# Kernel optimization log

Hardware: AMD Instinct MI355X
Metric: run time of the kernel (lower is better)

The kernel has to match this reference:

```python
import jax, jax.numpy as jnp
import numpy as np

IN_C = 256
OUT_C = 256
N = 100000
E = 3200000


def setup_inputs() -> dict:
    key = jax.random.key(0)
    ks = jax.random.split(key, 8)
    x = jax.random.normal(ks[0], (N, IN_C), dtype=jnp.float32)
    edge_index = jax.random.randint(ks[1], (2, E), 0, N, dtype=jnp.int64)
    # GCNConv weights (glorot-scale) and biases
    s1 = float(np.sqrt(2.0 / (IN_C + OUT_C)))
    s2 = float(np.sqrt(2.0 / (OUT_C + OUT_C)))
    W1 = jax.random.normal(ks[2], (IN_C, OUT_C), dtype=jnp.float32) * s1
    b1 = jnp.zeros((OUT_C,), dtype=jnp.float32)
    W2 = jax.random.normal(ks[3], (OUT_C, OUT_C), dtype=jnp.float32) * s2
    b2 = jnp.zeros((OUT_C,), dtype=jnp.float32)
    alpha = jnp.asarray(0.25, dtype=jnp.float32)  # PReLU default init
    return {"x": x, "edge_index": edge_index, "W1": W1, "b1": b1,
            "W2": W2, "b2": b2, "alpha": alpha}


def _gcn_aggregate(h, src, dst, norm, b, n):
    # message = norm_e * h[src_e]; scatter-add into dst; add bias
    msg = h[src] * norm[:, None]
    agg = jax.ops.segment_sum(msg, dst, num_segments=n)
    return agg + b


def reference(x, edge_index, W1, b1, W2, b2, alpha):
    n = x.shape[0]
    loops = jnp.arange(n, dtype=edge_index.dtype)
    src = jnp.concatenate([edge_index[0], loops])  # self-loops appended
    dst = jnp.concatenate([edge_index[1], loops])
    # symmetric degree normalization with self-loops (PyG GCNConv default)
    deg = jax.ops.segment_sum(jnp.ones_like(dst, dtype=x.dtype), dst, num_segments=n)
    dis = jnp.where(deg > 0, jax.lax.rsqrt(jnp.maximum(deg, 1e-12)), 0.0)
    norm = dis[src] * dis[dst]
    # layer 1: linear -> normalized scatter-aggregate -> PReLU
    h = _gcn_aggregate(x @ W1, src, dst, norm, b1, n)
    h = jnp.where(h >= 0, h, alpha * h)
    # layer 2 (last layer, no activation; batch=None -> node embeddings)
    h = _gcn_aggregate(h @ W2, src, dst, norm, b2, n)
    return h
```

## Files before the change

kernel.cpp:

```cpp
#include <hip/hip_runtime.h>
#include <cstdint>
#include <cstddef>


#define IN_C 256
#define BSHIFT 9
#define BCAP 24576

typedef __attribute__((ext_vector_type(8))) short bf16x8;
typedef __attribute__((ext_vector_type(4))) float f32x4;

__device__ __forceinline__ ushort f2bf(float x) {
    union { float f; uint32_t u; } v; v.f = x;
    uint32_t r = v.u + 0x7FFF + ((v.u >> 16) & 1);
    return (ushort)(r >> 16);
}
__device__ __forceinline__ float bf2f(ushort b) {
    union { uint32_t u; float f; } v; v.u = ((uint32_t)b) << 16;
    return v.f;
}

__global__ __launch_bounds__(256) void passA(const int* __restrict__ ei,
                                             int* __restrict__ bucketCnt,
                                             int2* __restrict__ bucketBuf, int E, int NB) {
    __shared__ int hist[256];
    __shared__ int gbase[256];
    __shared__ int cur[256];
    int tid = threadIdx.x;
    hist[tid] = 0; cur[tid] = 0;
    __syncthreads();
    int e0 = blockIdx.x * 4096;
    int src_r[16], dst_r[16];
#pragma unroll
    for (int i = 0; i < 16; ++i) {
        int e = e0 + i * 256 + tid;
        if (e < E) {
            src_r[i] = ei[e];
            dst_r[i] = ei[(size_t)E + e];
            atomicAdd(&hist[dst_r[i] >> BSHIFT], 1);
        } else dst_r[i] = -1;
    }
    __syncthreads();
    if (tid < NB && hist[tid] > 0) gbase[tid] = atomicAdd(&bucketCnt[tid], hist[tid]);
    __syncthreads();
#pragma unroll
    for (int i = 0; i < 16; ++i) {
        if (dst_r[i] >= 0) {
            int b = dst_r[i] >> BSHIFT;
            int p = atomicAdd(&cur[b], 1);
            int pos = gbase[b] + p;
            if (pos < BCAP) bucketBuf[(size_t)b * BCAP + pos] = make_int2(src_r[i], dst_r[i]);
        }
    }
}

__global__ void bucket_scan(const int* __restrict__ bucketCnt, int* __restrict__ bucket_base,
                            int* __restrict__ row_ptr, int NB, int N) {
    if (threadIdx.x == 0 && blockIdx.x == 0) {
        int run = 0;
        for (int b = 0; b < NB; ++b) {
            int c = bucketCnt[b]; if (c > BCAP) c = BCAP;
            bucket_base[b] = run; run += c;
        }
        row_ptr[N] = run;
    }
}

__global__ __launch_bounds__(256) void passB(const int2* __restrict__ bucketBuf,
                                             const int* __restrict__ bucketCnt,
                                             const int* __restrict__ bucket_base,
                                             int* __restrict__ row_ptr,
                                             int* __restrict__ csr_src, int N) {
    __shared__ int cnt[512];
    __shared__ int ofs[512];
    __shared__ int ssum[256];
    int b = blockIdx.x, tid = threadIdx.x;
    int base_node = b << BSHIFT;
    int nnodes = N - base_node; if (nnodes > 512) nnodes = 512;
    int nE = bucketCnt[b]; if (nE > BCAP) nE = BCAP;
    const int2* buf = bucketBuf + (size_t)b * BCAP;
    cnt[tid] = 0; cnt[tid + 256] = 0;
    __syncthreads();
    for (int i = tid; i < nE; i += 256) {
        int2 p = buf[i];
        atomicAdd(&cnt[p.y - base_node], 1);
    }
    __syncthreads();
    int c0 = cnt[2 * tid], c1 = cnt[2 * tid + 1];
    int s = c0 + c1;
    ssum[tid] = s;
    __syncthreads();
    for (int o = 1; o < 256; o <<= 1) {
        int add = (tid >= o) ? ssum[tid - o] : 0;
        __syncthreads();
        ssum[tid] += add;
        __syncthreads();
    }
    int run = ssum[tid] - s;
    int gb = bucket_base[b];
    int o0 = gb + run, o1 = gb + run + c0;
    ofs[2 * tid] = o0; ofs[2 * tid + 1] = o1;
    if (2 * tid < nnodes)     row_ptr[base_node + 2 * tid]     = o0;
    if (2 * tid + 1 < nnodes) row_ptr[base_node + 2 * tid + 1] = o1;
    __syncthreads();
    for (int i = tid; i < nE; i += 256) {
        int2 p = buf[i];
        int pos = atomicAdd(&ofs[p.y - base_node], 1);
        csr_src[pos] = p.x;
    }
}

__global__ __launch_bounds__(256) void dis2(const int* __restrict__ row_ptr,
                                            float* __restrict__ dis, int N) {
    int i = blockIdx.x * 256 + threadIdx.x;
    if (i < N) dis[i] = rsqrtf((float)(row_ptr[i + 1] - row_ptr[i] + 1));
}

__global__ __launch_bounds__(256) void split_x(const float* __restrict__ x,
                                               ushort* __restrict__ Xh,
                                               ushort* __restrict__ Xl, int total4) {
    int id = blockIdx.x * 256 + threadIdx.x;
    if (id >= total4) return;
    float4 v = ((const float4*)x)[id];
    ushort hx = f2bf(v.x), hy = f2bf(v.y), hz = f2bf(v.z), hw = f2bf(v.w);
    ((ushort4*)Xh)[id] = make_ushort4(hx, hy, hz, hw);
    ((ushort4*)Xl)[id] = make_ushort4(f2bf(v.x - bf2f(hx)), f2bf(v.y - bf2f(hy)),
                                      f2bf(v.z - bf2f(hz)), f2bf(v.w - bf2f(hw)));
}

__global__ __launch_bounds__(256) void prep_w(const float* __restrict__ W,
                                              ushort* __restrict__ WTh,
                                              ushort* __restrict__ WTl) {
    int id = blockIdx.x * 256 + threadIdx.x;
    int n = id >> 8, k = id & 255;
    float w = W[k * 256 + n];
    ushort h = f2bf(w);
    WTh[id] = h;
    WTl[id] = f2bf(w - bf2f(h));
}

__global__ __launch_bounds__(512, 2) void gemm_lds(const ushort* __restrict__ Ah,
                                                   const ushort* __restrict__ Al,
                                                   const ushort* __restrict__ Bh,
                                                   const ushort* __restrict__ Bl,
                                                   const float* __restrict__ dis,
                                                   ushort* __restrict__ C, int M) {
    __shared__ ushort Bsh[128][264];
    __shared__ ushort Bsl[128][264];
    int tid = threadIdx.x;
    int col0 = (blockIdx.x & 1) << 7;
    int brow = (blockIdx.x >> 1) << 9;
#pragma unroll
    for (int i = 0; i < 8; ++i) {
        int u = tid + i * 512;
        int cb = u >> 5, ko = (u & 31) * 8;
        *(bf16x8*)&Bsh[cb][ko] = *(const bf16x8*)&Bh[(size_t)(col0 + cb) * 256 + ko];
        *(bf16x8*)&Bsl[cb][ko] = *(const bf16x8*)&Bl[(size_t)(col0 + cb) * 256 + ko];
    }
    __syncthreads();

    int wave = tid >> 6, lane = tid & 63;
    int row0 = brow + wave * 64;
    if (row0 >= M) return;
    int lrow = lane & 15, lk = (lane >> 4) * 8;

    f32x4 acc[4][8];
#pragma unroll
    for (int i = 0; i < 4; ++i)
#pragma unroll
        for (int j = 0; j < 8; ++j) acc[i][j] = (f32x4)0.f;

#pragma unroll
    for (int ks = 0; ks < 8; ++ks) {
        int kb = ks * 32 + lk;
        bf16x8 ah[4], al[4];
#pragma unroll
        for (int i = 0; i < 4; ++i) {
            int row = row0 + i * 16 + lrow;
            if (row < M) {
                ah[i] = *(const bf16x8*)&Ah[(size_t)row * 256 + kb];
                al[i] = *(const bf16x8*)&Al[(size_t)row * 256 + kb];
            } else {
                ah[i] = (bf16x8)(short)0;
                al[i] = (bf16x8)(short)0;
            }
        }
#pragma unroll
        for (int j = 0; j < 8; ++j) {
            bf16x8 bh = *(bf16x8*)&Bsh[j * 16 + lrow][kb];
            bf16x8 bl = *(bf16x8*)&Bsl[j * 16 + lrow][kb];
#pragma unroll
            for (int i = 0; i < 4; ++i) {
                acc[i][j] = __builtin_amdgcn_mfma_f32_16x16x32_bf16(ah[i], bh, acc[i][j], 0, 0, 0);
                acc[i][j] = __builtin_amdgcn_mfma_f32_16x16x32_bf16(ah[i], bl, acc[i][j], 0, 0, 0);
                acc[i][j] = __builtin_amdgcn_mfma_f32_16x16x32_bf16(al[i], bh, acc[i][j], 0, 0, 0);
            }
        }
    }
    int rb = (lane >> 4) * 4;
#pragma unroll
    for (int i = 0; i < 4; ++i) {
#pragma unroll
        for (int r = 0; r < 4; ++r) {
            int row = row0 + i * 16 + rb + r;
            if (row >= M) continue;
            float dr = dis[row];
#pragma unroll
            for (int j = 0; j < 8; ++j) {
                int col = col0 + j * 16 + lrow;
                C[(size_t)row * 256 + col] = f2bf(dr * acc[i][j][r]);
            }
        }
    }
}

__global__ __launch_bounds__(256) void aggregate8(const ushort* __restrict__ Tp,
                                                  const int* __restrict__ row_ptr,
                                                  const int* __restrict__ csr_src,
                                                  const float* __restrict__ dis,
                                                  const float* __restrict__ bias,
                                                  const float* __restrict__ alpha_p,
                                                  float* __restrict__ outf,
                                                  ushort* __restrict__ outh,
                                                  ushort* __restrict__ outl,
                                                  int N, int mode) {
    int wave = threadIdx.x >> 6;
    int lane = threadIdx.x & 63;
    int n = blockIdx.x * 4 + wave;
    if (n >= N) return;
    int c = lane * 4;

    float ax[8], ay[8], az[8], aw[8];
#pragma unroll
    for (int t = 0; t < 8; ++t) { ax[t] = 0.f; ay[t] = 0.f; az[t] = 0.f; aw[t] = 0.f; }
    {
        ushort4 sv = *(const ushort4*)&Tp[(size_t)n * 256 + c];
        ax[0] = bf2f(sv.x); ay[0] = bf2f(sv.y); az[0] = bf2f(sv.z); aw[0] = bf2f(sv.w);
    }

    int e0 = row_ptr[n], e1 = row_ptr[n + 1];
    for (int base = e0; base < e1; base += 64) {
        int rem = e1 - base;
        int m = rem < 64 ? rem : 64;
        int idx = csr_src[base + (lane < m ? lane : 0)];
        int j = 0;
        for (; j + 8 <= m; j += 8) {
            int s[8];
            ushort4 v[8];
#pragma unroll
            for (int t = 0; t < 8; ++t) s[t] = __builtin_amdgcn_readlane(idx, j + t);
#pragma unroll
            for (int t = 0; t < 8; ++t) v[t] = *(const ushort4*)&Tp[(size_t)s[t] * 256 + c];
#pragma unroll
            for (int t = 0; t < 8; ++t) {
                ax[t] += bf2f(v[t].x); ay[t] += bf2f(v[t].y);
                az[t] += bf2f(v[t].z); aw[t] += bf2f(v[t].w);
            }
        }
        for (; j < m; ++j) {
            int s = __builtin_amdgcn_readlane(idx, j);
            ushort4 v = *(const ushort4*)&Tp[(size_t)s * 256 + c];
            ax[0] += bf2f(v.x); ay[0] += bf2f(v.y); az[0] += bf2f(v.z); aw[0] += bf2f(v.w);
        }
    }
#pragma unroll
    for (int t = 1; t < 8; ++t) { ax[0] += ax[t]; ay[0] += ay[t]; az[0] += az[t]; aw[0] += aw[t]; }

    float dn = dis[n];
    float4 bv = *(const float4*)&bias[c];
    float rx = dn * ax[0] + bv.x;
    float ry = dn * ay[0] + bv.y;
    float rz = dn * az[0] + bv.z;
    float rw = dn * aw[0] + bv.w;
    if (mode) {
        float al = *alpha_p;
        rx = rx >= 0.f ? rx : al * rx;
        ry = ry >= 0.f ? ry : al * ry;
        rz = rz >= 0.f ? rz : al * rz;
        rw = rw >= 0.f ? rw : al * rw;
        ushort hx = f2bf(rx), hy = f2bf(ry), hz = f2bf(rz), hw = f2bf(rw);
        *(ushort4*)&outh[(size_t)n * 256 + c] = make_ushort4(hx, hy, hz, hw);
        *(ushort4*)&outl[(size_t)n * 256 + c] = make_ushort4(f2bf(rx - bf2f(hx)), f2bf(ry - bf2f(hy)),
                                                             f2bf(rz - bf2f(hz)), f2bf(rw - bf2f(hw)));
    } else {
        f32x4 r; r.x = rx; r.y = ry; r.z = rz; r.w = rw;
        __builtin_nontemporal_store(r, (f32x4*)&outf[(size_t)n * 256 + c]);
    }
}

extern "C" void kernel_launch(void* const* d_in, const int* in_sizes, int n_in,
                              void* d_out, int out_size, void* d_ws, size_t ws_size,
                              hipStream_t stream) {
    const float* x = (const float*)d_in[0];
    const int* ei = (const int*)d_in[1];
    const float* W1 = (const float*)d_in[2];
    const float* b1 = (const float*)d_in[3];
    const float* W2 = (const float*)d_in[4];
    const float* b2 = (const float*)d_in[5];
    const float* alpha = (const float*)d_in[6];
    int N = in_sizes[0] / IN_C;
    int E = in_sizes[1] / 2;
    int NB = (N + 511) >> BSHIFT;
    if (NB > 256) return;

    char* ws = (char*)d_ws;
    size_t off = 0;
    auto alloc = [&](size_t bytes) {
        void* p = ws + off;
        off = (off + bytes + 255) & ~(size_t)255;
        return p;
    };
    int* row_ptr     = (int*)alloc(((size_t)N + 1) * 4);
    float* dis       = (float*)alloc((size_t)N * 4);
    int* csr_src     = (int*)alloc((size_t)E * 4);
    int* bucketCnt   = (int*)alloc(256 * 4);
    int* bucket_base = (int*)alloc(256 * 4);
    ushort* Tp       = (ushort*)alloc((size_t)N * IN_C * 2);
    ushort* Xl       = (ushort*)alloc((size_t)N * IN_C * 2);
    if (off > ws_size) return;
    int2* bucketBuf = (int2*)Tp;
    if ((size_t)NB * BCAP * 8 > (size_t)N * IN_C * 2) return;

    char* dob = (char*)d_out;
    ushort* Xh  = (ushort*)dob;
    ushort* W1h = (ushort*)(dob + (size_t)N * IN_C * 2);
    ushort* W1l = W1h + 65536;
    ushort* W2h = W1h + 131072;
    ushort* W2l = W1h + 196608;
    float* outf = (float*)d_out;

    hipMemsetAsync(bucketCnt, 0, 256 * 4, stream);

    passA<<<(E + 4095) / 4096, 256, 0, stream>>>(ei, bucketCnt, bucketBuf, E, NB);
    bucket_scan<<<1, 64, 0, stream>>>(bucketCnt, bucket_base, row_ptr, NB, N);
    passB<<<NB, 256, 0, stream>>>(bucketBuf, bucketCnt, bucket_base, row_ptr, csr_src, N);
    int nb256 = (N + 255) / 256;
    dis2<<<nb256, 256, 0, stream>>>(row_ptr, dis, N);

    int total4 = N * (IN_C / 4);
    split_x<<<(total4 + 255) / 256, 256, 0, stream>>>(x, Xh, Xl, total4);
    prep_w<<<256, 256, 0, stream>>>(W1, W1h, W1l);
    prep_w<<<256, 256, 0, stream>>>(W2, W2h, W2l);

    int gblocks = ((N + 511) / 512) * 2;
    int ablocks = (N + 3) / 4;

    gemm_lds<<<gblocks, 512, 0, stream>>>(Xh, Xl, W1h, W1l, dis, Tp, N);
    aggregate8<<<ablocks, 256, 0, stream>>>(Tp, row_ptr, csr_src, dis, b1, alpha,
                                            nullptr, Xh , Xl , N, 1);
    gemm_lds<<<gblocks, 512, 0, stream>>>(Xh , Xl , W2h, W2l, dis, Tp, N);
    aggregate8<<<ablocks, 256, 0, stream>>>(Tp, row_ptr, csr_src, dis, b2, alpha,
                                            outf, nullptr, nullptr, N, 0);
}
```

Baseline: 723.4 us.

## Fuse x bf16 split into first GEMM and merge small prep kernels

The first GEMM now reads fp32 x directly and splits each value into bf16 hi/lo parts in registers, so the separate split_x pass and its write and reread of two bf16 copies of x are gone. The degree-normalisation kernel is folded into passB, the single-thread bucket scan becomes a parallel 256-thread scan, and the two weight-prep launches are merged into one. The trade-off is that the GEMM's A-operand loads double in bytes (fp32 instead of bf16) and the conversion work is repeated per column-half block.

```diff
diff --git a/kernel.cpp b/kernel.cpp
--- a/kernel.cpp
+++ b/kernel.cpp
@@ -54,23 +54,31 @@
     }
 }
 
-__global__ void bucket_scan(const int* __restrict__ bucketCnt, int* __restrict__ bucket_base,
-                            int* __restrict__ row_ptr, int NB, int N) {
-    if (threadIdx.x == 0 && blockIdx.x == 0) {
-        int run = 0;
-        for (int b = 0; b < NB; ++b) {
-            int c = bucketCnt[b]; if (c > BCAP) c = BCAP;
-            bucket_base[b] = run; run += c;
-        }
-        row_ptr[N] = run;
-    }
+__global__ __launch_bounds__(256) void bucket_scanP(const int* __restrict__ bucketCnt,
+                                                    int* __restrict__ bucket_base,
+                                                    int* __restrict__ row_ptr, int NB, int N) {
+    __shared__ int sdata[256];
+    int tid = threadIdx.x;
+    int c = 0;
+    if (tid < NB) { c = bucketCnt[tid]; if (c > BCAP) c = BCAP; }
+    sdata[tid] = c;
+    __syncthreads();
+    for (int o = 1; o < 256; o <<= 1) {
+        int add = (tid >= o) ? sdata[tid - o] : 0;
+        __syncthreads();
+        sdata[tid] += add;
+        __syncthreads();
+    }
+    if (tid < NB) bucket_base[tid] = sdata[tid] - c;
+    if (tid == 255) row_ptr[N] = sdata[255];
 }
 
 __global__ __launch_bounds__(256) void passB(const int2* __restrict__ bucketBuf,
                                              const int* __restrict__ bucketCnt,
                                              const int* __restrict__ bucket_base,
                                              int* __restrict__ row_ptr,
-                                             int* __restrict__ csr_src, int N) {
+                                             int* __restrict__ csr_src,
+                                             float* __restrict__ dis, int N) {
     __shared__ int cnt[512];
     __shared__ int ofs[512];
     __shared__ int ssum[256];
@@ -100,8 +108,14 @@
     int gb = bucket_base[b];
     int o0 = gb + run, o1 = gb + run + c0;
     ofs[2 * tid] = o0; ofs[2 * tid + 1] = o1;
-    if (2 * tid < nnodes)     row_ptr[base_node + 2 * tid]     = o0;
-    if (2 * tid + 1 < nnodes) row_ptr[base_node + 2 * tid + 1] = o1;
+    if (2 * tid < nnodes) {
+        row_ptr[base_node + 2 * tid] = o0;
+        dis[base_node + 2 * tid] = rsqrtf((float)(c0 + 1));
+    }
+    if (2 * tid + 1 < nnodes) {
+        row_ptr[base_node + 2 * tid + 1] = o1;
+        dis[base_node + 2 * tid + 1] = rsqrtf((float)(c1 + 1));
+    }
     __syncthreads();
     for (int i = tid; i < nE; i += 256) {
         int2 p = buf[i];
@@ -110,33 +124,101 @@
     }
 }
 
-__global__ __launch_bounds__(256) void dis2(const int* __restrict__ row_ptr,
-                                            float* __restrict__ dis, int N) {
-    int i = blockIdx.x * 256 + threadIdx.x;
-    if (i < N) dis[i] = rsqrtf((float)(row_ptr[i + 1] - row_ptr[i] + 1));
-}
-
-__global__ __launch_bounds__(256) void split_x(const float* __restrict__ x,
-                                               ushort* __restrict__ Xh,
-                                               ushort* __restrict__ Xl, int total4) {
+__global__ __launch_bounds__(256) void prep_w2(const float* __restrict__ W1,
+                                               const float* __restrict__ W2,
+                                               ushort* __restrict__ W1h, ushort* __restrict__ W1l,
+                                               ushort* __restrict__ W2h, ushort* __restrict__ W2l) {
     int id = blockIdx.x * 256 + threadIdx.x;
-    if (id >= total4) return;
-    float4 v = ((const float4*)x)[id];
-    ushort hx = f2bf(v.x), hy = f2bf(v.y), hz = f2bf(v.z), hw = f2bf(v.w);
-    ((ushort4*)Xh)[id] = make_ushort4(hx, hy, hz, hw);
-    ((ushort4*)Xl)[id] = make_ushort4(f2bf(v.x - bf2f(hx)), f2bf(v.y - bf2f(hy)),
-                                      f2bf(v.z - bf2f(hz)), f2bf(v.w - bf2f(hw)));
-}
-
-__global__ __launch_bounds__(256) void prep_w(const float* __restrict__ W,
-                                              ushort* __restrict__ WTh,
-                                              ushort* __restrict__ WTl) {
-    int id = blockIdx.x * 256 + threadIdx.x;
-    int n = id >> 8, k = id & 255;
+    const float* W = (id < 65536) ? W1 : W2;
+    ushort* Th = (id < 65536) ? W1h : W2h;
+    ushort* Tl = (id < 65536) ? W1l : W2l;
+    int lid = id & 65535;
+    int n = lid >> 8, k = lid & 255;
     float w = W[k * 256 + n];
     ushort h = f2bf(w);
-    WTh[id] = h;
-    WTl[id] = f2bf(w - bf2f(h));
+    Th[lid] = h;
+    Tl[lid] = f2bf(w - bf2f(h));
+}
+
+__global__ __launch_bounds__(512, 2) void gemm_f32a(const float* __restrict__ A,
+                                                    const ushort* __restrict__ Bh,
+                                                    const ushort* __restrict__ Bl,
+                                                    const float* __restrict__ dis,
+                                                    ushort* __restrict__ C, int M) {
+    __shared__ ushort Bsh[128][264];
+    __shared__ ushort Bsl[128][264];
+    int tid = threadIdx.x;
+    int col0 = (blockIdx.x & 1) << 7;
+    int brow = (blockIdx.x >> 1) << 9;
+#pragma unroll
+    for (int i = 0; i < 8; ++i) {
+        int u = tid + i * 512;
+        int cb = u >> 5, ko = (u & 31) * 8;
+        *(bf16x8*)&Bsh[cb][ko] = *(const bf16x8*)&Bh[(size_t)(col0 + cb) * 256 + ko];
+        *(bf16x8*)&Bsl[cb][ko] = *(const bf16x8*)&Bl[(size_t)(col0 + cb) * 256 + ko];
+    }
+    __syncthreads();
+
+    int wave = tid >> 6, lane = tid & 63;
+    int row0 = brow + wave * 64;
+    if (row0 >= M) return;
+    int lrow = lane & 15, lk = (lane >> 4) * 8;
+
+    f32x4 acc[4][8];
+#pragma unroll
+    for (int i = 0; i < 4; ++i)
+#pragma unroll
+        for (int j = 0; j < 8; ++j) acc[i][j] = (f32x4)0.f;
+
+#pragma unroll
+    for (int ks = 0; ks < 8; ++ks) {
+        int kb = ks * 32 + lk;
+        bf16x8 ah[4], al[4];
+#pragma unroll
+        for (int i = 0; i < 4; ++i) {
+            int row = row0 + i * 16 + lrow;
+            if (row < M) {
+                float4 f0 = *(const float4*)&A[(size_t)row * 256 + kb];
+                float4 f1 = *(const float4*)&A[(size_t)row * 256 + kb + 4];
+                float f[8] = {f0.x, f0.y, f0.z, f0.w, f1.x, f1.y, f1.z, f1.w};
+#pragma unroll
+                for (int k = 0; k < 8; ++k) {
+                    ushort h = f2bf(f[k]);
+                    ah[i][k] = (short)h;
+                    al[i][k] = (short)f2bf(f[k] - bf2f(h));
+                }
+            } else {
+                ah[i] = (bf16x8)(short)0;
+                al[i] = (bf16x8)(short)0;
+            }
+        }
+#pragma unroll
+        for (int j = 0; j < 8; ++j) {
+            bf16x8 bh = *(bf16x8*)&Bsh[j * 16 + lrow][kb];
+            bf16x8 bl = *(bf16x8*)&Bsl[j * 16 + lrow][kb];
+#pragma unroll
+            for (int i = 0; i < 4; ++i) {
+                acc[i][j] = __builtin_amdgcn_mfma_f32_16x16x32_bf16(ah[i], bh, acc[i][j], 0, 0, 0);
+                acc[i][j] = __builtin_amdgcn_mfma_f32_16x16x32_bf16(ah[i], bl, acc[i][j], 0, 0, 0);
+                acc[i][j] = __builtin_amdgcn_mfma_f32_16x16x32_bf16(al[i], bh, acc[i][j], 0, 0, 0);
+            }
+        }
+    }
+    int rb = (lane >> 4) * 4;
+#pragma unroll
+    for (int i = 0; i < 4; ++i) {
+#pragma unroll
+        for (int r = 0; r < 4; ++r) {
+            int row = row0 + i * 16 + rb + r;
+            if (row >= M) continue;
+            float dr = dis[row];
+#pragma unroll
+            for (int j = 0; j < 8; ++j) {
+                int col = col0 + j * 16 + lrow;
+                C[(size_t)row * 256 + col] = f2bf(dr * acc[i][j][r]);
+            }
+        }
+    }
 }
 
 __global__ __launch_bounds__(512, 2) void gemm_lds(const ushort* __restrict__ Ah,
@@ -316,13 +398,13 @@
     int* bucketCnt   = (int*)alloc(256 * 4);
     int* bucket_base = (int*)alloc(256 * 4);
     ushort* Tp       = (ushort*)alloc((size_t)N * IN_C * 2);
-    ushort* Xl       = (ushort*)alloc((size_t)N * IN_C * 2);
+    ushort* Hl       = (ushort*)alloc((size_t)N * IN_C * 2);
     if (off > ws_size) return;
     int2* bucketBuf = (int2*)Tp;
     if ((size_t)NB * BCAP * 8 > (size_t)N * IN_C * 2) return;
 
     char* dob = (char*)d_out;
-    ushort* Xh  = (ushort*)dob;
+    ushort* Hh  = (ushort*)dob;
     ushort* W1h = (ushort*)(dob + (size_t)N * IN_C * 2);
     ushort* W1l = W1h + 65536;
     ushort* W2h = W1h + 131072;
@@ -332,23 +414,18 @@
     hipMemsetAsync(bucketCnt, 0, 256 * 4, stream);
 
     passA<<<(E + 4095) / 4096, 256, 0, stream>>>(ei, bucketCnt, bucketBuf, E, NB);
-    bucket_scan<<<1, 64, 0, stream>>>(bucketCnt, bucket_base, row_ptr, NB, N);
-    passB<<<NB, 256, 0, stream>>>(bucketBuf, bucketCnt, bucket_base, row_ptr, csr_src, N);
-    int nb256 = (N + 255) / 256;
-    dis2<<<nb256, 256, 0, stream>>>(row_ptr, dis, N);
-
-    int total4 = N * (IN_C / 4);
-    split_x<<<(total4 + 255) / 256, 256, 0, stream>>>(x, Xh, Xl, total4);
-    prep_w<<<256, 256, 0, stream>>>(W1, W1h, W1l);
-    prep_w<<<256, 256, 0, stream>>>(W2, W2h, W2l);
+    bucket_scanP<<<1, 256, 0, stream>>>(bucketCnt, bucket_base, row_ptr, NB, N);
+    passB<<<NB, 256, 0, stream>>>(bucketBuf, bucketCnt, bucket_base, row_ptr, csr_src, dis, N);
+
+    prep_w2<<<512, 256, 0, stream>>>(W1, W2, W1h, W1l, W2h, W2l);
 
     int gblocks = ((N + 511) / 512) * 2;
     int ablocks = (N + 3) / 4;
 
-    gemm_lds<<<gblocks, 512, 0, stream>>>(Xh, Xl, W1h, W1l, dis, Tp, N);
+    gemm_f32a<<<gblocks, 512, 0, stream>>>(x, W1h, W1l, dis, Tp, N);
     aggregate8<<<ablocks, 256, 0, stream>>>(Tp, row_ptr, csr_src, dis, b1, alpha,
-                                            nullptr, Xh , Xl , N, 1);
-    gemm_lds<<<gblocks, 512, 0, stream>>>(Xh , Xl , W2h, W2l, dis, Tp, N);
+                                            nullptr, Hh, Hl, N, 1);
+    gemm_lds<<<gblocks, 512, 0, stream>>>(Hh, Hl, W2h, W2l, dis, Tp, N);
     aggregate8<<<ablocks, 256, 0, stream>>>(Tp, row_ptr, csr_src, dis, b2, alpha,
                                             outf, nullptr, nullptr, N, 0);
 }
```

New measurement: 688.1 us. 4.9% less time.
